# Performance work log

Hardware: AMD Instinct MI355X
Metric: run time of the kernel (lower is better)

Reference implementation:

```python
import jax, jax.numpy as jnp
import numpy as np

B, S, D = 2, 2048, 1024   # batch, seq, d_model
E, K, H = 8, 4, 1024      # experts, top-k, expert hidden
SH = 2 * H                # shared-expert hidden (n_shared_experts=2)


def setup_inputs() -> dict:
    key = jax.random.key(0)
    ks = jax.random.split(key, 24)
    f = lambda k, shape: jax.random.normal(k, shape, dtype=jnp.float32) * 0.02
    return {
        "x": jax.random.normal(ks[0], (B, S, D), dtype=jnp.float32),
        # Linear(in_features, out_features), stored as [in, out]
        "lin0_w": f(ks[1], (D, D)), "lin0_b": f(ks[2], (D,)),
        "swi1_w1": f(ks[3], (D, D)), "swi1_b1": f(ks[4], (D,)),
        "swi1_w2": f(ks[5], (D, D)), "swi1_b2": f(ks[6], (D,)),
        # MoE router (no bias) + routed experts (SwiGLU FFN, no bias)
        "gate_w": f(ks[7], (E, D)),
        "exp_w1": f(ks[8], (E, D, H)),
        "exp_w3": f(ks[9], (E, D, H)),
        "exp_w2": f(ks[10], (E, H, D)),
        # shared experts fused into one wider SwiGLU MLP (2 shared experts)
        "sh_w1": f(ks[11], (D, SH)),
        "sh_w3": f(ks[12], (D, SH)),
        "sh_w2": f(ks[13], (SH, D)),
        # second Linear + SwiGLU block (num_ff=2)
        "lin1_w": f(ks[14], (D, D)), "lin1_b": f(ks[15], (D,)),
        "swi2_w1": f(ks[16], (D, D)), "swi2_b1": f(ks[17], (D,)),
        "swi2_w2": f(ks[18], (D, D)), "swi2_b2": f(ks[19], (D,)),
    }


def _silu(x):
    return x * jax.nn.sigmoid(x)


def _swiglu(x, w1, b1, w2, b2):
    return _silu(x @ w1 + b1) * (x @ w2 + b2)


def _moe(x, gate_w, exp_w1, exp_w3, exp_w2, sh_w1, sh_w3, sh_w2):
    b, s, d = x.shape
    t = b * s
    xt = x.reshape(t, d)
    # router: softmax scores, greedy top-k, normalized weights (scaling factor = 1)
    scores = jax.nn.softmax(xt @ gate_w.T, axis=-1)          # [T, E]
    topv, topi = jax.lax.top_k(scores, K)                    # [T, K]
    topv = topv / jnp.sum(topv, axis=-1, keepdims=True)
    combine = jnp.zeros((t, E), xt.dtype).at[jnp.arange(t)[:, None], topi].set(topv)  # [T, E]
    # routed experts: SwiGLU FFN per expert, dense-masked combine (same math as dispatch)
    g = _silu(jnp.einsum('td,edh->eth', xt, exp_w1))
    u = jnp.einsum('td,edh->eth', xt, exp_w3)
    yexp = jnp.einsum('eth,ehd->etd', g * u, exp_w2)         # [E, T, D]
    routed = jnp.einsum('te,etd->td', combine, yexp)         # [T, D]
    # shared experts (always on)
    shared = (_silu(xt @ sh_w1) * (xt @ sh_w3)) @ sh_w2      # [T, D]
    return (routed + shared).reshape(b, s, d)


def reference(x, lin0_w, lin0_b, swi1_w1, swi1_b1, swi1_w2, swi1_b2,
              gate_w, exp_w1, exp_w3, exp_w2, sh_w1, sh_w3, sh_w2,
              lin1_w, lin1_b, swi2_w1, swi2_b1, swi2_w2, swi2_b2):
    h = x @ lin0_w + lin0_b
    h = _swiglu(h, swi1_w1, swi1_b1, swi1_w2, swi1_b2)
    h = _moe(h, gate_w, exp_w1, exp_w3, exp_w2, sh_w1, sh_w3, sh_w2)
    h = h @ lin1_w + lin1_b
    h = _swiglu(h, swi2_w1, swi2_b1, swi2_w2, swi2_b2)
    return h
```

## Files before the change

### kernel.cpp

```cpp
#include <hip/hip_runtime.h>
#include <cstdint>
#include <cstddef>

#define T_TOKENS 4096
#define D_MODEL  1024
#define N_EXP    8
#define TOP_K    4
#define H_EXP    1024
#define SH_HID   2048
#define TK       (T_TOKENS*TOP_K)

typedef __bf16 bf16x8 __attribute__((ext_vector_type(8)));
typedef __bf16 bf16x4 __attribute__((ext_vector_type(4)));
typedef float  f32x4  __attribute__((ext_vector_type(4)));

__device__ __forceinline__ float silu_f(float x) {
    return x / (1.0f + expf(-x));
}

__device__ __forceinline__ void gload16(void* lds, const void* g)
{
    __builtin_amdgcn_global_load_lds(
        (const __attribute__((address_space(1))) unsigned int*)g,
        (__attribute__((address_space(3))) unsigned int*)lds,
        16, 0, 0);
}

template<int NT, bool SEG, bool GATHER, bool GLU>
__global__ __launch_bounds__(256)
void gemm_sp(const float* __restrict__ A, int lda,
             const float* __restrict__ W1, const float* __restrict__ W3,
             int64_t w_estride, int ldw,
             const float* __restrict__ bias1, const float* __restrict__ bias2,
             float* __restrict__ C, __bf16* __restrict__ Cb1, int ldc,
             int M, int Kd,
             const int* __restrict__ seg_off,
             const int* __restrict__ gather)
{
    constexpr int BM = 128, BN = 128, BK = 32;
    __shared__ __bf16 Asl[NT][BM * BK];
    __shared__ __bf16 Bsl[NT][BN * BK];

    int m0, m1, e = 0;
    if (SEG) {
        e = blockIdx.z;
        int s0 = seg_off[e], s1 = seg_off[e + 1];
        m0 = s0 + blockIdx.y * BM;
        if (m0 >= s1) return;
        m1 = (m0 + BM < s1) ? (m0 + BM) : s1;
    } else {
        m0 = blockIdx.y * BM;
        m1 = (m0 + BM < M) ? (m0 + BM) : M;
    }
    const int n0 = blockIdx.x * BN;

    const int tid  = threadIdx.x;
    const int lane = tid & 63;
    const int w    = tid >> 6;
    const int wm   = w >> 1, wn = w & 1;
    const int fr   = lane & 15, fq = lane >> 4;

    const float* aP[4]; int aR[4], aQ[4];
#pragma unroll
    for (int i = 0; i < 4; ++i) {
        int Li = tid + 256 * i;
        int r = Li >> 3, q = Li & 7;
        aR[i] = r; aQ[i] = q;
        int grow = m0 + r;
        if (grow > m1 - 1) grow = m1 - 1;
        if (GATHER) grow = gather[grow];
        aP[i] = A + (int64_t)grow * lda + q * 4;
    }

    const int bn  = tid & 127;
    const int bkh = tid >> 7;
    const float* Wsrc; int wcol;
    if (GLU) {
        int cl = n0 + bn;
        int B  = cl >> 4;
        Wsrc = (B & 1) ? W3 : W1;
        wcol = ((B >> 1) << 4) | (cl & 15);
    } else {
        Wsrc = W1; wcol = n0 + bn;
    }
    const float* Wb = Wsrc + (int64_t)e * w_estride + (int64_t)(bkh * 16) * ldw + wcol;

    f32x4 zero4 = {0.f, 0.f, 0.f, 0.f};
    f32x4 acc[4][4];
#pragma unroll
    for (int i = 0; i < 4; ++i)
#pragma unroll
        for (int j = 0; j < 4; ++j) acc[i][j] = zero4;

    float4 av[4];
    float  wv[16];

#define GLOADS(K0)                                                         \
    do {                                                                   \
        _Pragma("unroll")                                                  \
        for (int i = 0; i < 4; ++i)                                        \
            av[i] = *reinterpret_cast<const float4*>(aP[i] + (K0));        \
        _Pragma("unroll")                                                  \
        for (int j = 0; j < 16; ++j)                                       \
            wv[j] = Wb[(int64_t)((K0) + j) * ldw];                         \
    } while (0)

    const int nk = Kd / BK;
    GLOADS(0);

    for (int ks = 0; ks < nk; ++ks) {
        bf16x4 pa[NT][4];
        bf16x4 pw[NT][4];
#pragma unroll
        for (int i = 0; i < 4; ++i) {
            float vv[4] = {av[i].x, av[i].y, av[i].z, av[i].w};
#pragma unroll
            for (int t = 0; t < 4; ++t) {
                float v = vv[t];
                __bf16 h = (__bf16)v;
                pa[0][i][t] = h;
                if (NT >= 2) {
                    float r = v - (float)h;
                    if (NT == 2) {
                        pa[1][i][t] = (__bf16)r;
                    } else {
                        __bf16 m = (__bf16)r;
                        pa[1][i][t] = m;
                        pa[2][i][t] = (__bf16)(r - (float)m);
                    }
                }
            }
        }
#pragma unroll
        for (int qd = 0; qd < 4; ++qd) {
#pragma unroll
            for (int t = 0; t < 4; ++t) {
                float v = wv[qd * 4 + t];
                __bf16 h = (__bf16)v;
                pw[0][qd][t] = h;
                if (NT >= 2) {
                    float r = v - (float)h;
                    if (NT == 2) {
                        pw[1][qd][t] = (__bf16)r;
                    } else {
                        __bf16 m = (__bf16)r;
                        pw[1][qd][t] = m;
                        pw[2][qd][t] = (__bf16)(r - (float)m);
                    }
                }
            }
        }

        __syncthreads();
#pragma unroll
        for (int i = 0; i < 4; ++i) {
            int r = aR[i], q = aQ[i];
            int c = (q >> 1) ^ ((r >> 1) & 3);
            int idx = r * BK + c * 8 + (q & 1) * 4;
#pragma unroll
            for (int p = 0; p < NT; ++p)
                *reinterpret_cast<bf16x4*>(&Asl[p][idx]) = pa[p][i];
        }
#pragma unroll
        for (int qd = 0; qd < 4; ++qd) {
            int q32 = bkh * 4 + qd;
            int c = (q32 >> 1) ^ ((bn >> 1) & 3);
            int idx = bn * BK + c * 8 + (q32 & 1) * 4;
#pragma unroll
            for (int p = 0; p < NT; ++p)
                *reinterpret_cast<bf16x4*>(&Bsl[p][idx]) = pw[p][qd];
        }

        if (ks + 1 < nk) GLOADS((ks + 1) * BK);
        __syncthreads();

        bf16x8 bfr[NT][4];
#pragma unroll
        for (int p = 0; p < NT; ++p)
#pragma unroll
            for (int j = 0; j < 4; ++j) {
                int rown = wn * 64 + j * 16 + fr;
                int c = fq ^ ((rown >> 1) & 3);
                bfr[p][j] = *reinterpret_cast<const bf16x8*>(&Bsl[p][rown * BK + c * 8]);
            }
#pragma unroll
        for (int im = 0; im < 4; ++im) {
            bf16x8 af[NT];
            int rowm = wm * 64 + im * 16 + fr;
            int c = fq ^ ((rowm >> 1) & 3);
#pragma unroll
            for (int p = 0; p < NT; ++p)
                af[p] = *reinterpret_cast<const bf16x8*>(&Asl[p][rowm * BK + c * 8]);
#pragma unroll
            for (int jn = 0; jn < 4; ++jn) {
                f32x4 a = acc[im][jn];
                a = __builtin_amdgcn_mfma_f32_16x16x32_bf16(af[0], bfr[0][jn], a, 0, 0, 0);
                if (NT >= 2) {
                    a = __builtin_amdgcn_mfma_f32_16x16x32_bf16(af[0], bfr[1][jn], a, 0, 0, 0);
                    a = __builtin_amdgcn_mfma_f32_16x16x32_bf16(af[1], bfr[0][jn], a, 0, 0, 0);
                }
                if (NT == 3) {
                    a = __builtin_amdgcn_mfma_f32_16x16x32_bf16(af[1], bfr[1][jn], a, 0, 0, 0);
                    a = __builtin_amdgcn_mfma_f32_16x16x32_bf16(af[0], bfr[2][jn], a, 0, 0, 0);
                    a = __builtin_amdgcn_mfma_f32_16x16x32_bf16(af[2], bfr[0][jn], a, 0, 0, 0);
                }
                acc[im][jn] = a;
            }
        }
    }
#undef GLOADS

    if (GLU) {
#pragma unroll
        for (int jn = 0; jn < 4; jn += 2) {
            int gcol = (n0 >> 1) + wn * 32 + (jn >> 1) * 16 + fr;
            float bv1 = bias1 ? bias1[gcol] : 0.f;
            float bv2 = bias2 ? bias2[gcol] : 0.f;
#pragma unroll
            for (int im = 0; im < 4; ++im) {
                f32x4 v1 = acc[im][jn];
                f32x4 v2 = acc[im][jn + 1];
#pragma unroll
                for (int r = 0; r < 4; ++r) {
                    int grow = m0 + wm * 64 + im * 16 + fq * 4 + r;
                    if (grow < m1) {
                        float val = silu_f(v1[r] + bv1) * (v2[r] + bv2);
                        int64_t o = (int64_t)grow * ldc + gcol;
                        C[o] = val;
                        if (Cb1) Cb1[o] = (__bf16)val;
                    }
                }
            }
        }
    } else {
#pragma unroll
        for (int jn = 0; jn < 4; ++jn) {
            int col = n0 + wn * 64 + jn * 16 + fr;
            float bv = bias1 ? bias1[col] : 0.f;
#pragma unroll
            for (int im = 0; im < 4; ++im) {
                f32x4 v = acc[im][jn];
#pragma unroll
                for (int r = 0; r < 4; ++r) {
                    int grow = m0 + wm * 64 + im * 16 + fq * 4 + r;
                    if (grow < m1)
                        C[(int64_t)grow * ldc + col] = v[r] + bv;
                }
            }
        }
    }
}

template<bool SEG, bool GATHER, bool GLU, bool EMITB>
__global__ __launch_bounds__(256)
void gemm_gl(const __bf16* __restrict__ A, int lda,
             const __bf16* __restrict__ W1, const __bf16* __restrict__ W3,
             int64_t w_estride, int ldw,
             const float* __restrict__ bias1, const float* __restrict__ bias2,
             float* __restrict__ C, __bf16* __restrict__ Cb, int ldc,
             int M, int Kd,
             const int* __restrict__ seg_off,
             const int* __restrict__ gather)
{
    constexpr int BK = 32;
    __shared__ __bf16 Asl[2][128 * BK];
    __shared__ __bf16 Bsl[2][128 * BK];

    int m0, m1, e = 0;
    if (SEG) {
        e = blockIdx.z;
        int s0 = seg_off[e], s1 = seg_off[e + 1];
        m0 = s0 + blockIdx.y * 128;
        if (m0 >= s1) return;
        m1 = (m0 + 128 < s1) ? (m0 + 128) : s1;
    } else {
        m0 = blockIdx.y * 128;
        m1 = (m0 + 128 < M) ? (m0 + 128) : M;
    }
    const int n0 = blockIdx.x * 128;

    const int tid  = threadIdx.x;
    const int lane = tid & 63;
    const int w    = tid >> 6;
    const int wm   = w >> 1, wn = w & 1;
    const int fr   = lane & 15, fq = lane >> 4;

    const __bf16* As[2]; const __bf16* Ws[2];
    int ldsOff[2];
#pragma unroll
    for (int i = 0; i < 2; ++i) {
        int L = tid + 256 * i;
        int r = L >> 2, cp = L & 3;
        int cs = cp ^ ((r >> 1) & 3);
        ldsOff[i] = (i * 256 + w * 64) * 8;
        int grow = m0 + r;
        if (grow > m1 - 1) grow = m1 - 1;
        if (GATHER) grow = gather[grow];
        As[i] = A + (int64_t)grow * lda + cs * 8;
        int cl = n0 + r;
        const __bf16* base; int srcrow;
        if (GLU) {
            int B = cl >> 4;
            base = (B & 1) ? W3 : W1;
            srcrow = ((B >> 1) << 4) | (cl & 15);
        } else {
            base = W1; srcrow = cl;
        }
        Ws[i] = base + (int64_t)e * w_estride + (int64_t)srcrow * ldw + cs * 8;
    }

#define STAGE(buf, K0)                                                      \
    do {                                                                    \
        _Pragma("unroll")                                                   \
        for (int i = 0; i < 2; ++i) {                                       \
            gload16(&Asl[buf][ldsOff[i]], As[i] + (K0));                    \
            gload16(&Bsl[buf][ldsOff[i]], Ws[i] + (K0));                    \
        }                                                                   \
    } while (0)

    f32x4 zero4 = {0.f, 0.f, 0.f, 0.f};
    f32x4 acc[4][4];
#pragma unroll
    for (int i = 0; i < 4; ++i)
#pragma unroll
        for (int j = 0; j < 4; ++j) acc[i][j] = zero4;

    const int nk = Kd / BK;
    int cur = 0;
    STAGE(0, 0);
    __syncthreads();

    for (int ks = 0; ks < nk; ++ks) {
        if (ks + 1 < nk) STAGE(cur ^ 1, (ks + 1) * BK);

        bf16x8 bfr[4];
#pragma unroll
        for (int j = 0; j < 4; ++j) {
            int rown = wn * 64 + j * 16 + fr;
            int c = fq ^ ((rown >> 1) & 3);
            bfr[j] = *reinterpret_cast<const bf16x8*>(&Bsl[cur][rown * BK + c * 8]);
        }
#pragma unroll
        for (int im = 0; im < 4; ++im) {
            int rowm = wm * 64 + im * 16 + fr;
            int c = fq ^ ((rowm >> 1) & 3);
            bf16x8 af = *reinterpret_cast<const bf16x8*>(&Asl[cur][rowm * BK + c * 8]);
#pragma unroll
            for (int jn = 0; jn < 4; ++jn)
                acc[im][jn] = __builtin_amdgcn_mfma_f32_16x16x32_bf16(af, bfr[jn], acc[im][jn], 0, 0, 0);
        }
        __syncthreads();
        cur ^= 1;
    }
#undef STAGE

    if (GLU) {
#pragma unroll
        for (int jn = 0; jn < 4; jn += 2) {
            int gcol = (n0 >> 1) + wn * 32 + (jn >> 1) * 16 + fr;
            float bv1 = bias1 ? bias1[gcol] : 0.f;
            float bv2 = bias2 ? bias2[gcol] : 0.f;
#pragma unroll
            for (int im = 0; im < 4; ++im) {
                f32x4 v1 = acc[im][jn];
                f32x4 v2 = acc[im][jn + 1];
#pragma unroll
                for (int r = 0; r < 4; ++r) {
                    int grow = m0 + wm * 64 + im * 16 + fq * 4 + r;
                    if (grow < m1) {
                        float val = silu_f(v1[r] + bv1) * (v2[r] + bv2);
                        int64_t o = (int64_t)grow * ldc + gcol;
                        if (EMITB) Cb[o] = (__bf16)val;
                        else       C[o]  = val;
                    }
                }
            }
        }
    } else {
#pragma unroll
        for (int jn = 0; jn < 4; ++jn) {
            int col = n0 + wn * 64 + jn * 16 + fr;
            float bv = bias1 ? bias1[col] : 0.f;
#pragma unroll
            for (int im = 0; im < 4; ++im) {
                f32x4 v = acc[im][jn];
#pragma unroll
                for (int r = 0; r < 4; ++r) {
                    int grow = m0 + wm * 64 + im * 16 + fq * 4 + r;
                    if (grow < m1) {
                        int64_t o = (int64_t)grow * ldc + col;
                        if (EMITB) Cb[o] = (__bf16)(v[r] + bv);
                        else       C[o]  = v[r] + bv;
                    }
                }
            }
        }
    }
}

template<bool WBF, bool SEG, bool GATHER, bool GLU, bool EMITB>
__global__ __launch_bounds__(256)
void gemm_bb(const __bf16* __restrict__ A, int lda,
             const void* __restrict__ W1v, const void* __restrict__ W3v,
             int64_t w_estride, int ldw,
             const float* __restrict__ bias1, const float* __restrict__ bias2,
             float* __restrict__ C, __bf16* __restrict__ Cb, int ldc,
             int M, int Kd,
             const int* __restrict__ seg_off,
             const int* __restrict__ gather)
{
    constexpr int BK = 32;
    __shared__ __bf16 Asl[128 * BK];
    __shared__ __bf16 Bsl[128 * BK];

    int m0, m1, e = 0;
    if (SEG) {
        e = blockIdx.z;
        int s0 = seg_off[e], s1 = seg_off[e + 1];
        m0 = s0 + blockIdx.y * 128;
        if (m0 >= s1) return;
        m1 = (m0 + 128 < s1) ? (m0 + 128) : s1;
    } else {
        m0 = blockIdx.y * 128;
        m1 = (m0 + 128 < M) ? (m0 + 128) : M;
    }
    const int n0 = blockIdx.x * 128;

    const int tid  = threadIdx.x;
    const int lane = tid & 63;
    const int w    = tid >> 6;
    const int wm   = w >> 1, wn = w & 1;
    const int fr   = lane & 15, fq = lane >> 4;

    int aWr[2]; const __bf16* Ab[2];
#pragma unroll
    for (int i = 0; i < 2; ++i) {
        int L = tid + 256 * i;
        int r = L >> 2, ch = L & 3;
        aWr[i] = r * BK + (ch ^ ((r >> 1) & 3)) * 8;
        int grow = m0 + r;
        if (grow > m1 - 1) grow = m1 - 1;
        if (GATHER) grow = gather[grow];
        Ab[i] = A + (int64_t)grow * lda + ch * 8;
    }

    const int bn  = tid & 127;
    const int bkh = tid >> 7;
    int wcol; const void* Wsel;
    if (GLU) {
        int cl = n0 + bn;
        int B  = cl >> 4;
        Wsel = (B & 1) ? W3v : W1v;
        wcol = ((B >> 1) << 4) | (cl & 15);
    } else {
        Wsel = W1v; wcol = n0 + bn;
    }
    const float* Wbf = (const float*)Wsel + (int64_t)e * w_estride + (int64_t)(bkh * 16) * ldw + wcol;
    int wWrS[2];
#pragma unroll
    for (int c = 0; c < 2; ++c)
        wWrS[c] = bn * BK + ((bkh * 2 + c) ^ ((bn >> 1) & 3)) * 8;

    f32x4 zero4 = {0.f, 0.f, 0.f, 0.f};
    f32x4 acc[4][4];
#pragma unroll
    for (int i = 0; i < 4; ++i)
#pragma unroll
        for (int j = 0; j < 4; ++j) acc[i][j] = zero4;

    bf16x8 areg[2];
    bf16x8 wreg[2];

#define GLOADS(K0)                                                          \
    do {                                                                    \
        areg[0] = *reinterpret_cast<const bf16x8*>(Ab[0] + (K0));           \
        areg[1] = *reinterpret_cast<const bf16x8*>(Ab[1] + (K0));           \
        _Pragma("unroll")                                                   \
        for (int j = 0; j < 16; ++j)                                        \
            wreg[j >> 3][j & 7] = (__bf16)Wbf[(int64_t)((K0) + j) * ldw];   \
    } while (0)

    const int nk = Kd / BK;
    GLOADS(0);

    for (int ks = 0; ks < nk; ++ks) {
        __syncthreads();
        *reinterpret_cast<bf16x8*>(&Asl[aWr[0]]) = areg[0];
        *reinterpret_cast<bf16x8*>(&Asl[aWr[1]]) = areg[1];
        *reinterpret_cast<bf16x8*>(&Bsl[wWrS[0]]) = wreg[0];
        *reinterpret_cast<bf16x8*>(&Bsl[wWrS[1]]) = wreg[1];
        if (ks + 1 < nk) GLOADS((ks + 1) * BK);
        __syncthreads();

        bf16x8 bfr[4];
#pragma unroll
        for (int j = 0; j < 4; ++j) {
            int rown = wn * 64 + j * 16 + fr;
            int c = fq ^ ((rown >> 1) & 3);
            bfr[j] = *reinterpret_cast<const bf16x8*>(&Bsl[rown * BK + c * 8]);
        }
#pragma unroll
        for (int im = 0; im < 4; ++im) {
            int rowm = wm * 64 + im * 16 + fr;
            int c = fq ^ ((rowm >> 1) & 3);
            bf16x8 af = *reinterpret_cast<const bf16x8*>(&Asl[rowm * BK + c * 8]);
#pragma unroll
            for (int jn = 0; jn < 4; ++jn)
                acc[im][jn] = __builtin_amdgcn_mfma_f32_16x16x32_bf16(af, bfr[jn], acc[im][jn], 0, 0, 0);
        }
    }
#undef GLOADS

    if (GLU) {
#pragma unroll
        for (int jn = 0; jn < 4; jn += 2) {
            int gcol = (n0 >> 1) + wn * 32 + (jn >> 1) * 16 + fr;
            float bv1 = bias1 ? bias1[gcol] : 0.f;
            float bv2 = bias2 ? bias2[gcol] : 0.f;
#pragma unroll
            for (int im = 0; im < 4; ++im) {
                f32x4 v1 = acc[im][jn];
                f32x4 v2 = acc[im][jn + 1];
#pragma unroll
                for (int r = 0; r < 4; ++r) {
                    int grow = m0 + wm * 64 + im * 16 + fq * 4 + r;
                    if (grow < m1) {
                        float val = silu_f(v1[r] + bv1) * (v2[r] + bv2);
                        int64_t o = (int64_t)grow * ldc + gcol;
                        if (EMITB) Cb[o] = (__bf16)val;
                        else       C[o]  = val;
                    }
                }
            }
        }
    } else {
#pragma unroll
        for (int jn = 0; jn < 4; ++jn) {
            int col = n0 + wn * 64 + jn * 16 + fr;
            float bv = bias1 ? bias1[col] : 0.f;
#pragma unroll
            for (int im = 0; im < 4; ++im) {
                f32x4 v = acc[im][jn];
#pragma unroll
                for (int r = 0; r < 4; ++r) {
                    int grow = m0 + wm * 64 + im * 16 + fq * 4 + r;
                    if (grow < m1) {
                        int64_t o = (int64_t)grow * ldc + col;
                        if (EMITB) Cb[o] = (__bf16)(v[r] + bv);
                        else       C[o]  = v[r] + bv;
                    }
                }
            }
        }
    }
}

__global__ __launch_bounds__(256)
void f2bT(const float* __restrict__ src, __bf16* __restrict__ dst, int R, int C)
{
    __shared__ float t[32][33];
    const int64_t eoff = (int64_t)blockIdx.z * R * C;
    src += eoff; dst += eoff;
    const int c0 = blockIdx.x * 32, r0 = blockIdx.y * 32;
    const int tx = threadIdx.x & 31, ty = threadIdx.x >> 5;
#pragma unroll
    for (int i = 0; i < 4; ++i) {
        int r = r0 + ty + i * 8;
        t[ty + i * 8][tx] = src[(int64_t)r * C + c0 + tx];
    }
    __syncthreads();
#pragma unroll
    for (int i = 0; i < 4; ++i) {
        int c = c0 + ty + i * 8;
        dst[(int64_t)c * R + r0 + tx] = (__bf16)t[tx][ty + i * 8];
    }
}

__global__ __launch_bounds__(256)
void router_logits(const float* __restrict__ h1, const float* __restrict__ gw,
                   int* __restrict__ topi, float* __restrict__ topw,
                   unsigned char* __restrict__ emask)
{
    const int wave = threadIdx.x >> 6, lane = threadIdx.x & 63;
    const int t = blockIdx.x * 4 + wave;
    const float* x = h1 + (int64_t)t * D_MODEL;
    float part[N_EXP];
#pragma unroll
    for (int e = 0; e < N_EXP; ++e) part[e] = 0.f;
#pragma unroll 4
    for (int i = 0; i < D_MODEL / 64; ++i) {
        int d = lane + 64 * i;
        float xv = x[d];
#pragma unroll
        for (int e = 0; e < N_EXP; ++e)
            part[e] = fmaf(xv, gw[e * D_MODEL + d], part[e]);
    }
#pragma unroll
    for (int m = 32; m > 0; m >>= 1)
#pragma unroll
        for (int e = 0; e < N_EXP; ++e)
            part[e] += __shfl_xor(part[e], m, 64);

    if (lane == 0) {
        float p[N_EXP];
        float mx = -1e30f;
#pragma unroll
        for (int e = 0; e < N_EXP; ++e) mx = part[e] > mx ? part[e] : mx;
        float z = 0.f;
#pragma unroll
        for (int e = 0; e < N_EXP; ++e) { p[e] = expf(part[e] - mx); z += p[e]; }
#pragma unroll
        for (int e = 0; e < N_EXP; ++e) p[e] /= z;
        bool used[N_EXP];
#pragma unroll
        for (int e = 0; e < N_EXP; ++e) used[e] = false;
        int sel[TOP_K]; float sv[TOP_K]; float wsum = 0.f;
        unsigned m8 = 0;
        for (int k = 0; k < TOP_K; ++k) {
            int best = 0; float bvv = -1.f;
            for (int e = 0; e < N_EXP; ++e)
                if (!used[e] && p[e] > bvv) { bvv = p[e]; best = e; }
            used[best] = true; sel[k] = best; sv[k] = bvv; wsum += bvv;
            m8 |= 1u << best;
        }
        for (int k = 0; k < TOP_K; ++k) {
            int idx = t * TOP_K + k;
            topi[idx] = sel[k];
            topw[idx] = sv[k] / wsum;
        }
        emask[t] = (unsigned char)m8;
    }
}

__global__ __launch_bounds__(256)
void rank_local(const unsigned char* __restrict__ emask,
                const int* __restrict__ topi,
                int* __restrict__ pose, int* __restrict__ bh)
{
    const int b = blockIdx.x;
    const int t = b * 256 + threadIdx.x;
    const int wave = threadIdx.x >> 6, lane = threadIdx.x & 63;
    const unsigned m8 = emask[t];

    __shared__ int wcnt[4][N_EXP];
    __shared__ int wbase[4][N_EXP];
    int lrank[N_EXP];
#pragma unroll
    for (int e = 0; e < N_EXP; ++e) {
        unsigned long long bal = __ballot((m8 >> e) & 1u);
        lrank[e] = __popcll(bal & ((1ull << lane) - 1ull));
        if (lane == 0) wcnt[wave][e] = __popcll(bal);
    }
    __syncthreads();
    if (threadIdx.x < N_EXP) {
        int e = threadIdx.x; int a = 0;
        for (int wv = 0; wv < 4; ++wv) { wbase[wv][e] = a; a += wcnt[wv][e]; }
        bh[b * N_EXP + e] = a;
    }
    __syncthreads();
#pragma unroll
    for (int k = 0; k < TOP_K; ++k) {
        int e = topi[t * TOP_K + k];
        pose[t * TOP_K + k] = wbase[wave][e] + lrank[e];
    }
}

__global__ void scan16(const int* __restrict__ bh, int* __restrict__ bb,
                       int* __restrict__ off)
{
    __shared__ int tot[N_EXP];
    if (threadIdx.x < N_EXP) {
        int e = threadIdx.x; int a = 0;
        for (int b = 0; b < 16; ++b) { bb[b * N_EXP + e] = a; a += bh[b * N_EXP + e]; }
        tot[e] = a;
    }
    __syncthreads();
    if (threadIdx.x == 0) {
        int a = 0; off[0] = 0;
        for (int e = 0; e < N_EXP; ++e) { a += tot[e]; off[e + 1] = a; }
    }
}

__global__ __launch_bounds__(256)
void rank_final(const int* __restrict__ topi, const int* __restrict__ pose,
                const int* __restrict__ bb, const int* __restrict__ off,
                int* __restrict__ perm, int* __restrict__ slot_of)
{
    const int b = blockIdx.x;
    const int t = b * 256 + threadIdx.x;
#pragma unroll
    for (int k = 0; k < TOP_K; ++k) {
        int e = topi[t * TOP_K + k];
        int slot = off[e] + bb[b * N_EXP + e] + pose[t * TOP_K + k];
        perm[slot] = t;
        slot_of[t * TOP_K + k] = slot;
    }
}

template<bool YB>
__global__ __launch_bounds__(256)
void combine_k(const void* __restrict__ yv, const float* __restrict__ topw,
               const int* __restrict__ slot_of, float* __restrict__ h2,
               __bf16* __restrict__ h2b)
{
    int t = blockIdx.x;
    int64_t s[TOP_K]; float wgt[TOP_K];
#pragma unroll
    for (int k = 0; k < TOP_K; ++k) {
        s[k] = slot_of[t * TOP_K + k];
        wgt[k] = topw[t * TOP_K + k];
    }
    int64_t base4 = ((int64_t)t * D_MODEL) / 4 + threadIdx.x;
    float4 v = reinterpret_cast<const float4*>(h2)[base4];
#pragma unroll
    for (int k = 0; k < TOP_K; ++k) {
        float yy[4];
        if (YB) {
            bf16x4 yb = reinterpret_cast<const bf16x4*>((const __bf16*)yv)
                            [s[k] * (D_MODEL / 4) + threadIdx.x];
            yy[0] = (float)yb[0]; yy[1] = (float)yb[1];
            yy[2] = (float)yb[2]; yy[3] = (float)yb[3];
        } else {
            float4 yf = reinterpret_cast<const float4*>((const float*)yv)
                            [s[k] * (D_MODEL / 4) + threadIdx.x];
            yy[0] = yf.x; yy[1] = yf.y; yy[2] = yf.z; yy[3] = yf.w;
        }
        v.x = fmaf(wgt[k], yy[0], v.x);
        v.y = fmaf(wgt[k], yy[1], v.y);
        v.z = fmaf(wgt[k], yy[2], v.z);
        v.w = fmaf(wgt[k], yy[3], v.w);
    }
    if (h2b) {
        bf16x4 o;
        o[0] = (__bf16)v.x; o[1] = (__bf16)v.y;
        o[2] = (__bf16)v.z; o[3] = (__bf16)v.w;
        reinterpret_cast<bf16x4*>(h2b)[base4] = o;
    } else {
        reinterpret_cast<float4*>(h2)[base4] = v;
    }
}

extern "C" void kernel_launch(void* const* d_in, const int* in_sizes, int n_in,
                              void* d_out, int out_size, void* d_ws, size_t ws_size,
                              hipStream_t stream)
{
    const float* x      = (const float*)d_in[0];
    const float* lin0_w = (const float*)d_in[1];
    const float* lin0_b = (const float*)d_in[2];
    const float* s1w1   = (const float*)d_in[3];
    const float* s1b1   = (const float*)d_in[4];
    const float* s1w2   = (const float*)d_in[5];
    const float* s1b2   = (const float*)d_in[6];
    const float* gate_w = (const float*)d_in[7];
    const float* ew1    = (const float*)d_in[8];
    const float* ew3    = (const float*)d_in[9];
    const float* ew2    = (const float*)d_in[10];
    const float* shw1   = (const float*)d_in[11];
    const float* shw3   = (const float*)d_in[12];
    const float* shw2   = (const float*)d_in[13];
    const float* lin1_w = (const float*)d_in[14];
    const float* lin1_b = (const float*)d_in[15];
    const float* s2w1   = (const float*)d_in[16];
    const float* s2b1   = (const float*)d_in[17];
    const float* s2w2   = (const float*)d_in[18];
    const float* s2b2   = (const float*)d_in[19];
    float* out = (float*)d_out;

    char* ws = (char*)d_ws;
    const size_t MB = 1024 * 1024;
    dim3 blk(256);
    const int64_t ES = (int64_t)D_MODEL * H_EXP;
    const bool full = ws_size >= (size_t)216 * MB;

    float* h0 = (float*)(ws + 0 * MB);
    float* h1 = (float*)(ws + 16 * MB);
    float* h2 = (float*)(ws + 32 * MB);

    if (full) {
        __bf16* yexp_b = (__bf16*)(ws + 48 * MB);
        __bf16* gu_b   = (__bf16*)(ws + 80 * MB);
        __bf16* gsh_b  = gu_b;
        __bf16* h1b    = (__bf16*)(ws + 112 * MB);
        __bf16* h2b    = (__bf16*)(ws + 120 * MB);
        __bf16* h3b    = (__bf16*)(ws + 128 * MB);
        __bf16* e1T = (__bf16*)(ws + 136 * MB);
        __bf16* e3T = (__bf16*)(ws + 152 * MB);
        __bf16* e2T = (__bf16*)(ws + 168 * MB);
        __bf16* s1T = (__bf16*)(ws + 184 * MB);
        __bf16* s3T = (__bf16*)(ws + 188 * MB);
        __bf16* s2T = (__bf16*)(ws + 192 * MB);
        __bf16* l1T = (__bf16*)(ws + 196 * MB);
        __bf16* q1T = (__bf16*)(ws + 198 * MB);
        __bf16* q2T = (__bf16*)(ws + 200 * MB);
        char* sm = ws + 202 * MB;
        int*   topi    = (int*)(sm);
        float* topw    = (float*)(sm + 64 * 1024);
        int*   pose    = (int*)(sm + 128 * 1024);
        int*   slot_of = (int*)(sm + 192 * 1024);
        int*   perm    = (int*)(sm + 256 * 1024);
        int*   bh      = (int*)(sm + 320 * 1024);
        int*   bb      = (int*)(sm + 321 * 1024);
        int*   off     = (int*)(sm + 322 * 1024);
        unsigned char* emask = (unsigned char*)(sm + 323 * 1024);

        f2bT<<<dim3(32, 32, N_EXP), blk, 0, stream>>>(ew1, e1T, D_MODEL, H_EXP);
        f2bT<<<dim3(32, 32, N_EXP), blk, 0, stream>>>(ew3, e3T, D_MODEL, H_EXP);
        f2bT<<<dim3(32, 32, N_EXP), blk, 0, stream>>>(ew2, e2T, H_EXP, D_MODEL);
        f2bT<<<dim3(64, 32, 1), blk, 0, stream>>>(shw1, s1T, D_MODEL, SH_HID);
        f2bT<<<dim3(64, 32, 1), blk, 0, stream>>>(shw3, s3T, D_MODEL, SH_HID);
        f2bT<<<dim3(32, 64, 1), blk, 0, stream>>>(shw2, s2T, SH_HID, D_MODEL);
        f2bT<<<dim3(32, 32, 1), blk, 0, stream>>>(lin1_w, l1T, D_MODEL, D_MODEL);
        f2bT<<<dim3(32, 32, 1), blk, 0, stream>>>(s2w1, q1T, D_MODEL, D_MODEL);
        f2bT<<<dim3(32, 32, 1), blk, 0, stream>>>(s2w2, q2T, D_MODEL, D_MODEL);

        gemm_sp<3, false, false, false><<<dim3(8, 32, 1), blk, 0, stream>>>(
            x, D_MODEL, lin0_w, nullptr, 0, D_MODEL, lin0_b, nullptr,
            h0, nullptr, D_MODEL, T_TOKENS, D_MODEL, nullptr, nullptr);

        gemm_sp<3, false, false, true><<<dim3(16, 32, 1), blk, 0, stream>>>(
            h0, D_MODEL, s1w1, s1w2, 0, D_MODEL, s1b1, s1b2,
            h1, h1b, D_MODEL, T_TOKENS, D_MODEL, nullptr, nullptr);

        router_logits<<<T_TOKENS / 4, blk, 0, stream>>>(h1, gate_w, topi, topw, emask);
        rank_local<<<16, blk, 0, stream>>>(emask, topi, pose, bh);
        scan16<<<1, 64, 0, stream>>>(bh, bb, off);
        rank_final<<<16, blk, 0, stream>>>(topi, pose, bb, off, perm, slot_of);

        gemm_gl<true, true, true, true><<<dim3(16, 128, N_EXP), blk, 0, stream>>>(
            h1b, D_MODEL, e1T, e3T, ES, D_MODEL, nullptr, nullptr,
            nullptr, gu_b, H_EXP, 0, D_MODEL, off, perm);
        gemm_gl<true, false, false, true><<<dim3(8, 128, N_EXP), blk, 0, stream>>>(
            gu_b, H_EXP, e2T, nullptr, ES, H_EXP, nullptr, nullptr,
            nullptr, yexp_b, D_MODEL, 0, H_EXP, off, nullptr);
        gemm_gl<false, false, true, true><<<dim3(32, 32, 1), blk, 0, stream>>>(
            h1b, D_MODEL, s1T, s3T, 0, D_MODEL, nullptr, nullptr,
            nullptr, gsh_b, SH_HID, T_TOKENS, D_MODEL, nullptr, nullptr);
        gemm_gl<false, false, false, false><<<dim3(8, 32, 1), blk, 0, stream>>>(
            gsh_b, SH_HID, s2T, nullptr, 0, SH_HID, nullptr, nullptr,
            h2, nullptr, D_MODEL, T_TOKENS, SH_HID, nullptr, nullptr);

        combine_k<true><<<T_TOKENS, blk, 0, stream>>>(yexp_b, topw, slot_of, h2, h2b);

        gemm_gl<false, false, false, true><<<dim3(8, 32, 1), blk, 0, stream>>>(
            h2b, D_MODEL, l1T, nullptr, 0, D_MODEL, lin1_b, nullptr,
            nullptr, h3b, D_MODEL, T_TOKENS, D_MODEL, nullptr, nullptr);

        gemm_gl<false, false, true, false><<<dim3(16, 32, 1), blk, 0, stream>>>(
            h3b, D_MODEL, q1T, q2T, 0, D_MODEL, s2b1, s2b2,
            out, nullptr, D_MODEL, T_TOKENS, D_MODEL, nullptr, nullptr);
    } else {
        float* yexp  = (float*)(ws + 48 * MB);
        __bf16* gu_b = (__bf16*)(ws + 112 * MB);
        __bf16* gsh_b = gu_b;
        __bf16* h1b  = (__bf16*)(ws + 144 * MB);
        char* sm = ws + 152 * MB;
        int*   topi    = (int*)(sm);
        float* topw    = (float*)(sm + 64 * 1024);
        int*   pose    = (int*)(sm + 128 * 1024);
        int*   slot_of = (int*)(sm + 192 * 1024);
        int*   perm    = (int*)(sm + 256 * 1024);
        int*   bh      = (int*)(sm + 320 * 1024);
        int*   bb      = (int*)(sm + 321 * 1024);
        int*   off     = (int*)(sm + 322 * 1024);
        unsigned char* emask = (unsigned char*)(sm + 323 * 1024);

        gemm_sp<3, false, false, false><<<dim3(8, 32, 1), blk, 0, stream>>>(
            x, D_MODEL, lin0_w, nullptr, 0, D_MODEL, lin0_b, nullptr,
            h0, nullptr, D_MODEL, T_TOKENS, D_MODEL, nullptr, nullptr);
        gemm_sp<3, false, false, true><<<dim3(16, 32, 1), blk, 0, stream>>>(
            h0, D_MODEL, s1w1, s1w2, 0, D_MODEL, s1b1, s1b2,
            h1, h1b, D_MODEL, T_TOKENS, D_MODEL, nullptr, nullptr);

        router_logits<<<T_TOKENS / 4, blk, 0, stream>>>(h1, gate_w, topi, topw, emask);
        rank_local<<<16, blk, 0, stream>>>(emask, topi, pose, bh);
        scan16<<<1, 64, 0, stream>>>(bh, bb, off);
        rank_final<<<16, blk, 0, stream>>>(topi, pose, bb, off, perm, slot_of);

        gemm_bb<false, true, true, true, true><<<dim3(16, 128, N_EXP), blk, 0, stream>>>(
            h1b, D_MODEL, ew1, ew3, ES, H_EXP, nullptr, nullptr,
            nullptr, gu_b, H_EXP, 0, D_MODEL, off, perm);
        gemm_bb<false, true, false, false, false><<<dim3(8, 128, N_EXP), blk, 0, stream>>>(
            gu_b, H_EXP, ew2, nullptr, (int64_t)H_EXP * D_MODEL, D_MODEL, nullptr, nullptr,
            yexp, nullptr, D_MODEL, 0, H_EXP, off, nullptr);
        gemm_bb<false, false, false, true, true><<<dim3(32, 32, 1), blk, 0, stream>>>(
            h1b, D_MODEL, shw1, shw3, 0, SH_HID, nullptr, nullptr,
            nullptr, gsh_b, SH_HID, T_TOKENS, D_MODEL, nullptr, nullptr);
        gemm_bb<false, false, false, false, false><<<dim3(8, 32, 1), blk, 0, stream>>>(
            gsh_b, SH_HID, shw2, nullptr, 0, D_MODEL, nullptr, nullptr,
            h2, nullptr, D_MODEL, T_TOKENS, SH_HID, nullptr, nullptr);

        combine_k<false><<<T_TOKENS, blk, 0, stream>>>(yexp, topw, slot_of, h2, nullptr);

        gemm_sp<2, false, false, false><<<dim3(8, 32, 1), blk, 0, stream>>>(
            h2, D_MODEL, lin1_w, nullptr, 0, D_MODEL, lin1_b, nullptr,
            h0, nullptr, D_MODEL, T_TOKENS, D_MODEL, nullptr, nullptr);
        gemm_sp<2, false, false, true><<<dim3(16, 32, 1), blk, 0, stream>>>(
            h0, D_MODEL, s2w1, s2w2, 0, D_MODEL, s2b1, s2b2,
            out, nullptr, D_MODEL, T_TOKENS, D_MODEL, nullptr, nullptr);
    }
}
```

Baseline: 609.6 us.

## Replace LDS-direct GEMM with 256x128 tile register-staged GEMM for bf16 paths

Replaces the global_load_lds double-buffered 128x128 GEMM with a kernel that uses 256x128 tiles and stages loads through registers into a single LDS buffer, with two barriers per K step. Each wave now computes 128x64 outputs (8x4 MFMA tiles), which raises weight reuse per block and halves the grid in M. It also adds a bf16-weight path to gemm_bb. The cost is higher register pressure, fewer blocks, coarser tails on uneven expert segments, and the loss of the async double-buffered loads.

```diff
diff --git a/kernel.cpp b/kernel.cpp
--- a/kernel.cpp
+++ b/kernel.cpp
@@ -16,14 +16,6 @@
 
 __device__ __forceinline__ float silu_f(float x) {
     return x / (1.0f + expf(-x));
-}
-
-__device__ __forceinline__ void gload16(void* lds, const void* g)
-{
-    __builtin_amdgcn_global_load_lds(
-        (const __attribute__((address_space(1))) unsigned int*)g,
-        (__attribute__((address_space(3))) unsigned int*)lds,
-        16, 0, 0);
 }
 
 template<int NT, bool SEG, bool GATHER, bool GLU>
@@ -253,7 +245,7 @@
 
 template<bool SEG, bool GATHER, bool GLU, bool EMITB>
 __global__ __launch_bounds__(256)
-void gemm_gl(const __bf16* __restrict__ A, int lda,
+void gemm_bt(const __bf16* __restrict__ A, int lda,
              const __bf16* __restrict__ W1, const __bf16* __restrict__ W3,
              int64_t w_estride, int ldw,
              const float* __restrict__ bias1, const float* __restrict__ bias2,
@@ -262,22 +254,22 @@
              const int* __restrict__ seg_off,
              const int* __restrict__ gather)
 {
-    constexpr int BK = 32;
-    __shared__ __bf16 Asl[2][128 * BK];
-    __shared__ __bf16 Bsl[2][128 * BK];
+    constexpr int BM = 256, BN = 128, BK = 32;
+    __shared__ __bf16 Asl[BM * BK];
+    __shared__ __bf16 Bsl[BN * BK];
 
     int m0, m1, e = 0;
     if (SEG) {
         e = blockIdx.z;
         int s0 = seg_off[e], s1 = seg_off[e + 1];
-        m0 = s0 + blockIdx.y * 128;
+        m0 = s0 + blockIdx.y * BM;
         if (m0 >= s1) return;
-        m1 = (m0 + 128 < s1) ? (m0 + 128) : s1;
+        m1 = (m0 + BM < s1) ? (m0 + BM) : s1;
     } else {
-        m0 = blockIdx.y * 128;
-        m1 = (m0 + 128 < M) ? (m0 + 128) : M;
-    }
-    const int n0 = blockIdx.x * 128;
+        m0 = blockIdx.y * BM;
+        m1 = (m0 + BM < M) ? (m0 + BM) : M;
+    }
+    const int n0 = blockIdx.x * BN;
 
     const int tid  = threadIdx.x;
     const int lane = tid & 63;
@@ -285,19 +277,25 @@
     const int wm   = w >> 1, wn = w & 1;
     const int fr   = lane & 15, fq = lane >> 4;
 
-    const __bf16* As[2]; const __bf16* Ws[2];
-    int ldsOff[2];
-#pragma unroll
-    for (int i = 0; i < 2; ++i) {
+    int aWr[4]; const __bf16* Ab[4];
+#pragma unroll
+    for (int i = 0; i < 4; ++i) {
         int L = tid + 256 * i;
-        int r = L >> 2, cp = L & 3;
-        int cs = cp ^ ((r >> 1) & 3);
-        ldsOff[i] = (i * 256 + w * 64) * 8;
+        int r = L >> 2, ch = L & 3;
+        aWr[i] = r * BK + (ch ^ ((r >> 1) & 3)) * 8;
         int grow = m0 + r;
         if (grow > m1 - 1) grow = m1 - 1;
         if (GATHER) grow = gather[grow];
-        As[i] = A + (int64_t)grow * lda + cs * 8;
-        int cl = n0 + r;
+        Ab[i] = A + (int64_t)grow * lda + ch * 8;
+    }
+
+    int wR[2]; const __bf16* Wt[2];
+#pragma unroll
+    for (int i = 0; i < 2; ++i) {
+        int L = tid + 256 * i;
+        int nl = L >> 2, ch = L & 3;
+        wR[i] = nl * BK + (ch ^ ((nl >> 1) & 3)) * 8;
+        int cl = n0 + nl;
         const __bf16* base; int srcrow;
         if (GLU) {
             int B = cl >> 4;
@@ -306,53 +304,61 @@
         } else {
             base = W1; srcrow = cl;
         }
-        Ws[i] = base + (int64_t)e * w_estride + (int64_t)srcrow * ldw + cs * 8;
-    }
-
-#define STAGE(buf, K0)                                                      \
+        Wt[i] = base + (int64_t)e * w_estride + (int64_t)srcrow * ldw + ch * 8;
+    }
+
+    f32x4 zero4 = {0.f, 0.f, 0.f, 0.f};
+    f32x4 acc[8][4];
+#pragma unroll
+    for (int i = 0; i < 8; ++i)
+#pragma unroll
+        for (int j = 0; j < 4; ++j) acc[i][j] = zero4;
+
+    bf16x8 areg[4];
+    bf16x8 wreg[2];
+
+#define GLOADS(K0)                                                          \
     do {                                                                    \
         _Pragma("unroll")                                                   \
-        for (int i = 0; i < 2; ++i) {                                       \
-            gload16(&Asl[buf][ldsOff[i]], As[i] + (K0));                    \
-            gload16(&Bsl[buf][ldsOff[i]], Ws[i] + (K0));                    \
-        }                                                                   \
+        for (int i = 0; i < 4; ++i)                                         \
+            areg[i] = *reinterpret_cast<const bf16x8*>(Ab[i] + (K0));       \
+        _Pragma("unroll")                                                   \
+        for (int i = 0; i < 2; ++i)                                         \
+            wreg[i] = *reinterpret_cast<const bf16x8*>(Wt[i] + (K0));       \
     } while (0)
 
-    f32x4 zero4 = {0.f, 0.f, 0.f, 0.f};
-    f32x4 acc[4][4];
-#pragma unroll
-    for (int i = 0; i < 4; ++i)
-#pragma unroll
-        for (int j = 0; j < 4; ++j) acc[i][j] = zero4;
-
     const int nk = Kd / BK;
-    int cur = 0;
-    STAGE(0, 0);
-    __syncthreads();
+    GLOADS(0);
 
     for (int ks = 0; ks < nk; ++ks) {
-        if (ks + 1 < nk) STAGE(cur ^ 1, (ks + 1) * BK);
+        __syncthreads();
+#pragma unroll
+        for (int i = 0; i < 4; ++i)
+            *reinterpret_cast<bf16x8*>(&Asl[aWr[i]]) = areg[i];
+#pragma unroll
+        for (int i = 0; i < 2; ++i)
+            *reinterpret_cast<bf16x8*>(&Bsl[wR[i]]) = wreg[i];
+        if (ks + 1 < nk) GLOADS((ks + 1) * BK);
+        __syncthreads();
 
         bf16x8 bfr[4];
 #pragma unroll
         for (int j = 0; j < 4; ++j) {
             int rown = wn * 64 + j * 16 + fr;
             int c = fq ^ ((rown >> 1) & 3);
-            bfr[j] = *reinterpret_cast<const bf16x8*>(&Bsl[cur][rown * BK + c * 8]);
-        }
-#pragma unroll
-        for (int im = 0; im < 4; ++im) {
-            int rowm = wm * 64 + im * 16 + fr;
+            bfr[j] = *reinterpret_cast<const bf16x8*>(&Bsl[rown * BK + c * 8]);
+        }
+#pragma unroll
+        for (int im = 0; im < 8; ++im) {
+            int rowm = wm * 128 + im * 16 + fr;
             int c = fq ^ ((rowm >> 1) & 3);
-            bf16x8 af = *reinterpret_cast<const bf16x8*>(&Asl[cur][rowm * BK + c * 8]);
+            bf16x8 af = *reinterpret_cast<const bf16x8*>(&Asl[rowm * BK + c * 8]);
 #pragma unroll
             for (int jn = 0; jn < 4; ++jn)
                 acc[im][jn] = __builtin_amdgcn_mfma_f32_16x16x32_bf16(af, bfr[jn], acc[im][jn], 0, 0, 0);
         }
-        __syncthreads();
-        cur ^= 1;
-    }
-#undef STAGE
+    }
+#undef GLOADS
 
     if (GLU) {
 #pragma unroll
@@ -361,12 +367,12 @@
             float bv1 = bias1 ? bias1[gcol] : 0.f;
             float bv2 = bias2 ? bias2[gcol] : 0.f;
 #pragma unroll
-            for (int im = 0; im < 4; ++im) {
+            for (int im = 0; im < 8; ++im) {
                 f32x4 v1 = acc[im][jn];
                 f32x4 v2 = acc[im][jn + 1];
 #pragma unroll
                 for (int r = 0; r < 4; ++r) {
-                    int grow = m0 + wm * 64 + im * 16 + fq * 4 + r;
+                    int grow = m0 + wm * 128 + im * 16 + fq * 4 + r;
                     if (grow < m1) {
                         float val = silu_f(v1[r] + bv1) * (v2[r] + bv2);
                         int64_t o = (int64_t)grow * ldc + gcol;
@@ -382,11 +388,11 @@
             int col = n0 + wn * 64 + jn * 16 + fr;
             float bv = bias1 ? bias1[col] : 0.f;
 #pragma unroll
-            for (int im = 0; im < 4; ++im) {
+            for (int im = 0; im < 8; ++im) {
                 f32x4 v = acc[im][jn];
 #pragma unroll
                 for (int r = 0; r < 4; ++r) {
-                    int grow = m0 + wm * 64 + im * 16 + fq * 4 + r;
+                    int grow = m0 + wm * 128 + im * 16 + fq * 4 + r;
                     if (grow < m1) {
                         int64_t o = (int64_t)grow * ldc + col;
                         if (EMITB) Cb[o] = (__bf16)(v[r] + bv);
@@ -444,22 +450,45 @@
         Ab[i] = A + (int64_t)grow * lda + ch * 8;
     }
 
-    const int bn  = tid & 127;
-    const int bkh = tid >> 7;
-    int wcol; const void* Wsel;
-    if (GLU) {
-        int cl = n0 + bn;
-        int B  = cl >> 4;
-        Wsel = (B & 1) ? W3v : W1v;
-        wcol = ((B >> 1) << 4) | (cl & 15);
+    int wR[2]; const __bf16* Wt[2];
+    const float* Wbf = nullptr;
+    int wWrS[2];
+    if (WBF) {
+#pragma unroll
+        for (int i = 0; i < 2; ++i) {
+            int L = tid + 256 * i;
+            int nl = L >> 2, ch = L & 3;
+            wR[i] = nl * BK + (ch ^ ((nl >> 1) & 3)) * 8;
+            int cl = n0 + nl;
+            const __bf16* base;
+            int srcrow;
+            if (GLU) {
+                int B = cl >> 4;
+                base = (const __bf16*)((B & 1) ? W3v : W1v);
+                srcrow = ((B >> 1) << 4) | (cl & 15);
+            } else {
+                base = (const __bf16*)W1v;
+                srcrow = cl;
+            }
+            Wt[i] = base + (int64_t)e * w_estride + (int64_t)srcrow * ldw + ch * 8;
+        }
     } else {
-        Wsel = W1v; wcol = n0 + bn;
-    }
-    const float* Wbf = (const float*)Wsel + (int64_t)e * w_estride + (int64_t)(bkh * 16) * ldw + wcol;
-    int wWrS[2];
-#pragma unroll
-    for (int c = 0; c < 2; ++c)
-        wWrS[c] = bn * BK + ((bkh * 2 + c) ^ ((bn >> 1) & 3)) * 8;
+        const int bn  = tid & 127;
+        const int bkh = tid >> 7;
+        int wcol; const void* Wsel;
+        if (GLU) {
+            int cl = n0 + bn;
+            int B  = cl >> 4;
+            Wsel = (B & 1) ? W3v : W1v;
+            wcol = ((B >> 1) << 4) | (cl & 15);
+        } else {
+            Wsel = W1v; wcol = n0 + bn;
+        }
+        Wbf = (const float*)Wsel + (int64_t)e * w_estride + (int64_t)(bkh * 16) * ldw + wcol;
+#pragma unroll
+        for (int c = 0; c < 2; ++c)
+            wWrS[c] = bn * BK + ((bkh * 2 + c) ^ ((bn >> 1) & 3)) * 8;
+    }
 
     f32x4 zero4 = {0.f, 0.f, 0.f, 0.f};
     f32x4 acc[4][4];
@@ -475,9 +504,14 @@
     do {                                                                    \
         areg[0] = *reinterpret_cast<const bf16x8*>(Ab[0] + (K0));           \
         areg[1] = *reinterpret_cast<const bf16x8*>(Ab[1] + (K0));           \
-        _Pragma("unroll")                                                   \
-        for (int j = 0; j < 16; ++j)                                        \
-            wreg[j >> 3][j & 7] = (__bf16)Wbf[(int64_t)((K0) + j) * ldw];   \
+        if (WBF) {                                                          \
+            wreg[0] = *reinterpret_cast<const bf16x8*>(Wt[0] + (K0));       \
+            wreg[1] = *reinterpret_cast<const bf16x8*>(Wt[1] + (K0));       \
+        } else {                                                            \
+            _Pragma("unroll")                                               \
+            for (int j = 0; j < 16; ++j)                                    \
+                wreg[j >> 3][j & 7] = (__bf16)Wbf[(int64_t)((K0) + j) * ldw]; \
+        }                                                                   \
     } while (0)
 
     const int nk = Kd / BK;
@@ -487,8 +521,13 @@
         __syncthreads();
         *reinterpret_cast<bf16x8*>(&Asl[aWr[0]]) = areg[0];
         *reinterpret_cast<bf16x8*>(&Asl[aWr[1]]) = areg[1];
-        *reinterpret_cast<bf16x8*>(&Bsl[wWrS[0]]) = wreg[0];
-        *reinterpret_cast<bf16x8*>(&Bsl[wWrS[1]]) = wreg[1];
+        if (WBF) {
+            *reinterpret_cast<bf16x8*>(&Bsl[wR[0]]) = wreg[0];
+            *reinterpret_cast<bf16x8*>(&Bsl[wR[1]]) = wreg[1];
+        } else {
+            *reinterpret_cast<bf16x8*>(&Bsl[wWrS[0]]) = wreg[0];
+            *reinterpret_cast<bf16x8*>(&Bsl[wWrS[1]]) = wreg[1];
+        }
         if (ks + 1 < nk) GLOADS((ks + 1) * BK);
         __syncthreads();
 
@@ -772,17 +811,16 @@
     const int64_t ES = (int64_t)D_MODEL * H_EXP;
     const bool full = ws_size >= (size_t)216 * MB;
 
-    float* h0 = (float*)(ws + 0 * MB);
-    float* h1 = (float*)(ws + 16 * MB);
-    float* h2 = (float*)(ws + 32 * MB);
-
     if (full) {
+        float*  h0 = (float*)(ws + 0 * MB);
+        float*  h1 = (float*)(ws + 16 * MB);
+        float*  h2 = (float*)(ws + 32 * MB);
         __bf16* yexp_b = (__bf16*)(ws + 48 * MB);
         __bf16* gu_b   = (__bf16*)(ws + 80 * MB);
         __bf16* gsh_b  = gu_b;
-        __bf16* h1b    = (__bf16*)(ws + 112 * MB);
-        __bf16* h2b    = (__bf16*)(ws + 120 * MB);
-        __bf16* h3b    = (__bf16*)(ws + 128 * MB);
+        __bf16* h1b = (__bf16*)(ws + 112 * MB);
+        __bf16* h2b = (__bf16*)(ws + 120 * MB);
+        __bf16* h3b = (__bf16*)(ws + 128 * MB);
         __bf16* e1T = (__bf16*)(ws + 136 * MB);
         __bf16* e3T = (__bf16*)(ws + 152 * MB);
         __bf16* e2T = (__bf16*)(ws + 168 * MB);
@@ -826,29 +864,32 @@
         scan16<<<1, 64, 0, stream>>>(bh, bb, off);
         rank_final<<<16, blk, 0, stream>>>(topi, pose, bb, off, perm, slot_of);
 
-        gemm_gl<true, true, true, true><<<dim3(16, 128, N_EXP), blk, 0, stream>>>(
+        gemm_bt<true, true, true, true><<<dim3(16, 64, N_EXP), blk, 0, stream>>>(
             h1b, D_MODEL, e1T, e3T, ES, D_MODEL, nullptr, nullptr,
             nullptr, gu_b, H_EXP, 0, D_MODEL, off, perm);
-        gemm_gl<true, false, false, true><<<dim3(8, 128, N_EXP), blk, 0, stream>>>(
+        gemm_bt<true, false, false, true><<<dim3(8, 64, N_EXP), blk, 0, stream>>>(
             gu_b, H_EXP, e2T, nullptr, ES, H_EXP, nullptr, nullptr,
             nullptr, yexp_b, D_MODEL, 0, H_EXP, off, nullptr);
-        gemm_gl<false, false, true, true><<<dim3(32, 32, 1), blk, 0, stream>>>(
+        gemm_bt<false, false, true, true><<<dim3(32, 16, 1), blk, 0, stream>>>(
             h1b, D_MODEL, s1T, s3T, 0, D_MODEL, nullptr, nullptr,
             nullptr, gsh_b, SH_HID, T_TOKENS, D_MODEL, nullptr, nullptr);
-        gemm_gl<false, false, false, false><<<dim3(8, 32, 1), blk, 0, stream>>>(
+        gemm_bt<false, false, false, false><<<dim3(8, 16, 1), blk, 0, stream>>>(
             gsh_b, SH_HID, s2T, nullptr, 0, SH_HID, nullptr, nullptr,
             h2, nullptr, D_MODEL, T_TOKENS, SH_HID, nullptr, nullptr);
 
         combine_k<true><<<T_TOKENS, blk, 0, stream>>>(yexp_b, topw, slot_of, h2, h2b);
 
-        gemm_gl<false, false, false, true><<<dim3(8, 32, 1), blk, 0, stream>>>(
+        gemm_bt<false, false, false, true><<<dim3(8, 16, 1), blk, 0, stream>>>(
             h2b, D_MODEL, l1T, nullptr, 0, D_MODEL, lin1_b, nullptr,
             nullptr, h3b, D_MODEL, T_TOKENS, D_MODEL, nullptr, nullptr);
 
-        gemm_gl<false, false, true, false><<<dim3(16, 32, 1), blk, 0, stream>>>(
+        gemm_bt<false, false, true, false><<<dim3(16, 16, 1), blk, 0, stream>>>(
             h3b, D_MODEL, q1T, q2T, 0, D_MODEL, s2b1, s2b2,
             out, nullptr, D_MODEL, T_TOKENS, D_MODEL, nullptr, nullptr);
     } else {
+        float* h0 = (float*)(ws + 0 * MB);
+        float* h1 = (float*)(ws + 16 * MB);
+        float* h2 = (float*)(ws + 32 * MB);
         float* yexp  = (float*)(ws + 48 * MB);
         __bf16* gu_b = (__bf16*)(ws + 112 * MB);
         __bf16* gsh_b = gu_b;
```

New measurement: 758.8 us. +24.5%, slower.
